# Optimization experiments

Measured on AMD Instinct MI355X. Metric: run time of the kernel, lower is better.

## Reference

```python
import jax, jax.numpy as jnp
import numpy as np

T = 2048      # num_tokens == max_seq_len
D = 4096      # d_in
H = 32        # num_heads
G = 8         # num_kv_groups
HD = 128      # head_dim
GS = H // G   # group_size = 4
EPS = 1e-6


def _make_rope(t, hd):
    inv_freq = 1.0 / (10000.0 ** (np.arange(0, hd, 2, dtype=np.float64) / hd))
    freqs = np.outer(np.arange(t, dtype=np.float64), inv_freq)      # [T, HD/2]
    emb = np.concatenate([freqs, freqs], axis=-1)                   # [T, HD]
    return (jnp.asarray(np.cos(emb), jnp.float32),
            jnp.asarray(np.sin(emb), jnp.float32))


def setup_inputs() -> dict:
    key = jax.random.key(0)
    ks = jax.random.split(key, 6)
    x = jax.random.normal(ks[0], (T, D), jnp.float32)
    # causal mask: True = masked (upper triangle above diagonal)
    mask = jnp.triu(jnp.ones((T, T), jnp.bool_), k=1)
    cos, sin = _make_rope(T, HD)
    s = 0.02
    Wq = jax.random.normal(ks[1], (D, H * HD), jnp.float32) * s
    Wk = jax.random.normal(ks[2], (D, G * HD), jnp.float32) * s
    Wv = jax.random.normal(ks[3], (D, G * HD), jnp.float32) * s
    Wo = jax.random.normal(ks[4], (H * HD, D), jnp.float32) * s
    qn_w = jnp.ones((HD,), jnp.float32)
    kn_w = jnp.ones((HD,), jnp.float32)
    return {"x": x, "mask": mask, "cos": cos, "sin": sin,
            "Wq": Wq, "Wk": Wk, "Wv": Wv, "Wo": Wo,
            "qn_w": qn_w, "kn_w": kn_w}


def _rmsnorm(u, w):
    # normalize over head_dim (last axis), eps inside sqrt
    var = jnp.mean(jnp.square(u), axis=-1, keepdims=True)
    return u * jax.lax.rsqrt(var + EPS) * w


def _rope(u, cos, sin):
    # rotate-half RoPE; u: [heads, T, HD], cos/sin: [T, HD]
    hd = u.shape[-1]
    u1, u2 = u[..., : hd // 2], u[..., hd // 2:]
    rot = jnp.concatenate([-u2, u1], axis=-1)
    return u * cos[None] + rot * sin[None]


def reference(x, mask, cos, sin, Wq, Wk, Wv, Wo, qn_w, kn_w):
    t = x.shape[0]
    q = (x @ Wq).reshape(t, H, HD).transpose(1, 0, 2)   # [H, T, HD]
    k = (x @ Wk).reshape(t, G, HD).transpose(1, 0, 2)   # [G, T, HD]
    v = (x @ Wv).reshape(t, G, HD).transpose(1, 0, 2)   # [G, T, HD]
    q = _rmsnorm(q, qn_w)
    k = _rmsnorm(k, kn_w)
    q = _rope(q, cos, sin)
    k = _rope(k, cos, sin)
    # GQA expansion: repeat_interleave along head axis
    k = jnp.repeat(k, GS, axis=0)                       # [H, T, HD]
    v = jnp.repeat(v, GS, axis=0)                       # [H, T, HD]
    scores = jnp.einsum('hqd,hkd->hqk', q, k) / (HD ** 0.5)
    scores = jnp.where(mask[None], -jnp.inf, scores)
    w = jax.nn.softmax(scores, axis=-1)
    attn = jnp.einsum('hqk,hkd->hqd', w, v)             # [H, T, HD]
    attn = attn.transpose(1, 0, 2).reshape(t, H * HD)
    return attn @ Wo
```

## Files before the change

### kernel.cpp

```cpp
#include <hip/hip_runtime.h>

#define T_ 2048
#define D_ 4096
#define H_ 32
#define G_ 8
#define HD_ 128

typedef float f32x4 __attribute__((ext_vector_type(4)));
typedef __bf16 bf16x8 __attribute__((ext_vector_type(8)));
typedef unsigned short u16x8 __attribute__((ext_vector_type(8)));
typedef unsigned short u16x4 __attribute__((ext_vector_type(4)));

__device__ __forceinline__ unsigned short f2bf(float f) {
  unsigned u = __builtin_bit_cast(unsigned, f);
  u += 0x7FFFu + ((u >> 16) & 1u);
  return (unsigned short)(u >> 16);
}
__device__ __forceinline__ float bf2f(unsigned short h) {
  return __builtin_bit_cast(float, (unsigned)h << 16);
}

__device__ __forceinline__ void gload_lds16(const unsigned short* g, unsigned short* l) {
  __builtin_amdgcn_global_load_lds((const __attribute__((address_space(1))) void*)g,
                                   (__attribute__((address_space(3))) void*)l, 16, 0, 0);
}

__global__ __launch_bounds__(256) void convert_bf16(const float* __restrict__ in,
                                                    unsigned short* __restrict__ out) {
  const size_t i = ((size_t)blockIdx.x * 256 + threadIdx.x) * 8;
  float4 a = *(const float4*)(in + i);
  float4 b = *(const float4*)(in + i + 4);
  u16x8 o;
  o[0] = f2bf(a.x); o[1] = f2bf(a.y); o[2] = f2bf(a.z); o[3] = f2bf(a.w);
  o[4] = f2bf(b.x); o[5] = f2bf(b.y); o[6] = f2bf(b.z); o[7] = f2bf(b.w);
  *(u16x8*)(out + i) = o;
}

__global__ __launch_bounds__(256) void transpose_convert(const float* __restrict__ Wm,
                                                         unsigned short* __restrict__ Wt,
                                                         int R, int C) {
  __shared__ float tile[64][65];
  const int r0 = blockIdx.x * 64, c0 = blockIdx.y * 64;
  const int lr4 = threadIdx.x >> 6, lc = threadIdx.x & 63;
#pragma unroll
  for (int i = 0; i < 16; ++i) {
    int r = i * 4 + lr4;
    tile[r][lc] = Wm[(size_t)(r0 + r) * C + c0 + lc];
  }
  __syncthreads();
#pragma unroll
  for (int i = 0; i < 16; ++i) {
    int r = i * 4 + lr4;
    Wt[(size_t)(c0 + r) * R + r0 + lc] = f2bf(tile[lc][r]);
  }
}

__global__ __launch_bounds__(256) void transpose_v(const unsigned short* __restrict__ v,
                                                   unsigned short* __restrict__ vt, int stride) {
  __shared__ unsigned short tile[64][65];
  const int t0 = blockIdx.x * 64, d0 = blockIdx.y * 64, g = blockIdx.z;
  const int lr4 = threadIdx.x >> 6, lc = threadIdx.x & 63;
#pragma unroll
  for (int i = 0; i < 16; ++i) {
    int r = i * 4 + lr4;
    tile[r][lc] = v[(size_t)(t0 + r) * stride + g * HD_ + d0 + lc];
  }
  __syncthreads();
#pragma unroll
  for (int i = 0; i < 16; ++i) {
    int r = i * 4 + lr4;
    vt[((size_t)g * HD_ + d0 + r) * T_ + t0 + lc] = tile[lc][r];
  }
}

__global__ __launch_bounds__(256) void norm_rope(const unsigned short* __restrict__ raw,
                                                 int stride,
                                                 unsigned short* __restrict__ outp,
                                                 const float* __restrict__ w,
                                                 const float* __restrict__ cs,
                                                 const float* __restrict__ sn, int NH) {
  const int row = blockIdx.x * 4 + (threadIdx.x >> 6);
  const int lane = threadIdx.x & 63;
  const int t = row / NH, h = row - t * NH;
  const unsigned short* src = raw + (size_t)t * stride + h * HD_;
  float u1 = bf2f(src[lane]);
  float u2 = bf2f(src[lane + 64]);
  float ss = u1 * u1 + u2 * u2;
#pragma unroll
  for (int m = 1; m < 64; m <<= 1) ss += __shfl_xor(ss, m);
  float rr = rsqrtf(ss * (1.f / 128.f) + 1e-6f);
  float c = cs[(size_t)t * HD_ + lane];
  float s = sn[(size_t)t * HD_ + lane];
  float a = u1 * rr * w[lane];
  float b = u2 * rr * w[lane + 64];
  unsigned short* dst = outp + ((size_t)h * T_ + t) * HD_;
  dst[lane]      = f2bf(a * c - b * s);
  dst[lane + 64] = f2bf(b * c + a * s);
}

template <int NF, int MQ, int F0, int F1>
__device__ __forceinline__ void mfma_g(f32x4 (&acc)[2][4][NF], bf16x8 (&af)[4][2],
                                       bf16x8 (&bf)[NF][2]) {
  __builtin_amdgcn_s_setprio(1);
#pragma unroll
  for (int fm = 0; fm < 4; ++fm)
#pragma unroll
    for (int fn = F0; fn < F1; ++fn) {
      f32x4 a = acc[MQ][fm][fn];
      a = __builtin_amdgcn_mfma_f32_16x16x32_bf16(af[fm][0], bf[fn][0], a, 0, 0, 0);
      a = __builtin_amdgcn_mfma_f32_16x16x32_bf16(af[fm][1], bf[fn][1], a, 0, 0, 0);
      acc[MQ][fm][fn] = a;
    }
  __builtin_amdgcn_s_setprio(0);
}

template <int NF, int OUTF32>
__global__ __launch_bounds__(512, 2) void gemm2(const unsigned short* __restrict__ A,
                                                const unsigned short* __restrict__ Bt,
                                                void* __restrict__ Cv, int M, int N,
                                                int K, int LDA) {
  constexpr int BN = NF * 64;
  constexpr int BBUF = NF * 4096;
  __shared__ __align__(16) unsigned short lds[32768 + 2 * BBUF];
  const int tid = threadIdx.x;
  const int wid = tid >> 6, lane = tid & 63;
  const int lr = lane & 15, lhi = lane >> 4;
  const int wr = wid >> 2, wcn = wid & 3;
  const int wr64 = wr * 64;

  int flat = blockIdx.y * gridDim.x + blockIdx.x;
  int nwg = gridDim.x * gridDim.y;
  int swz = (flat & 7) * (nwg >> 3) + (flat >> 3);
  const int brow = (swz & 7) * 256;
  const int bcol = (swz >> 3) * BN;

  const int nt = K >> 6;

  f32x4 acc[2][4][NF];
#pragma unroll
  for (int a = 0; a < 2; ++a)
#pragma unroll
    for (int b = 0; b < 4; ++b)
#pragma unroll
      for (int c = 0; c < NF; ++c) acc[a][b][c] = (f32x4){0.f, 0.f, 0.f, 0.f};

  const int t8 = tid >> 3;
  const int srcCol = ((tid & 7) ^ (t8 & 7)) * 8;
  auto stageA = [&](int d, int u, int ktp) {
    gload_lds16(A + (size_t)(brow + u * 64 + t8) * LDA + ktp * 64 + srcCol,
                &lds[d * 16384 + u * 4096 + tid * 8]);
  };
  auto stageB = [&](int d, int v, int ktp) {
    gload_lds16(Bt + (size_t)(bcol + v * 64 + t8) * LDA + ktp * 64 + srcCol,
                &lds[32768 + d * BBUF + v * 4096 + tid * 8]);
  };

  bf16x8 af[4][2], bf[NF][2];
  auto readA = [&](int d, int mq) {
#pragma unroll
    for (int fm = 0; fm < 4; ++fm) {
      int row = mq * 128 + wr64 + fm * 16 + lr;
      int base = d * 16384 + row * 64;
      int sw = (row & 7) << 3;
      af[fm][0] = *(const bf16x8*)&lds[base + ((lhi * 8) ^ sw)];
      af[fm][1] = *(const bf16x8*)&lds[base + ((32 + lhi * 8) ^ sw)];
    }
  };
  auto readBf = [&](int d, int fn, bf16x8 (&slot)[2]) {
    int row = wcn * (16 * NF) + fn * 16 + lr;
    int base = 32768 + d * BBUF + row * 64;
    int sw = (row & 7) << 3;
    slot[0] = *(const bf16x8*)&lds[base + ((lhi * 8) ^ sw)];
    slot[1] = *(const bf16x8*)&lds[base + ((32 + lhi * 8) ^ sw)];
  };

  stageA(0, 0, 0); stageA(0, 1, 0); stageA(0, 2, 0); stageA(0, 3, 0);
#pragma unroll
  for (int v = 0; v < NF; ++v) stageB(0, v, 0);
  stageA(1, 0, 1); stageA(1, 1, 1);
  asm volatile("s_waitcnt vmcnt(2)" ::: "memory");
  __builtin_amdgcn_s_barrier();

  for (int t = 0; t < nt; ++t) {
    const int d = t & 1, dn = d ^ 1;
    if constexpr (NF == 2) {
      readA(d, 0); readBf(d, 0, bf[0]); readBf(d, 1, bf[1]);
      if (t + 1 < nt) { stageA(dn, 2, t + 1); stageA(dn, 3, t + 1);
                        stageB(dn, 0, t + 1); stageB(dn, 1, t + 1); }
      __builtin_amdgcn_s_barrier();
      mfma_g<NF, 0, 0, 2>(acc, af, bf);
      __builtin_amdgcn_s_barrier();
      readA(d, 1);
      if (t + 2 < nt) { stageA(d, 0, t + 2); stageA(d, 1, t + 2); }
      __builtin_amdgcn_s_barrier();
      mfma_g<NF, 1, 0, 2>(acc, af, bf);
      if (t < nt - 2) asm volatile("s_waitcnt vmcnt(2)" ::: "memory");
      else if (t == nt - 2) asm volatile("s_waitcnt vmcnt(0)" ::: "memory");
      __builtin_amdgcn_s_barrier();
    } else {
      readA(d, 0); readBf(d, 0, bf[0]); readBf(d, 1, bf[1]);
      if (t + 1 < nt) { stageA(dn, 2, t + 1); stageA(dn, 3, t + 1); }
      __builtin_amdgcn_s_barrier();
      mfma_g<NF, 0, 0, 2>(acc, af, bf);
      __builtin_amdgcn_s_barrier();
      readBf(d, 2, bf[2]);
      if (t + 1 < nt) { stageB(dn, 0, t + 1); stageB(dn, 1, t + 1); stageB(dn, 2, t + 1); }
      __builtin_amdgcn_s_barrier();
      mfma_g<NF, 0, 2, 3>(acc, af, bf);
      __builtin_amdgcn_s_barrier();
      readA(d, 1);
      if (t + 2 < nt) { stageA(d, 0, t + 2); stageA(d, 1, t + 2); }
      __builtin_amdgcn_s_barrier();
      mfma_g<NF, 1, 0, 2>(acc, af, bf);
      __builtin_amdgcn_s_barrier();
      mfma_g<NF, 1, 2, 3>(acc, af, bf);
      if (t < nt - 2) asm volatile("s_waitcnt vmcnt(2)" ::: "memory");
      else if (t == nt - 2) asm volatile("s_waitcnt vmcnt(0)" ::: "memory");
      __builtin_amdgcn_s_barrier();
    }
  }

#pragma unroll
  for (int mq = 0; mq < 2; ++mq)
#pragma unroll
    for (int fm = 0; fm < 4; ++fm)
#pragma unroll
      for (int fn = 0; fn < NF; ++fn) {
        int col = bcol + wcn * (16 * NF) + fn * 16 + lr;
#pragma unroll
        for (int r = 0; r < 4; ++r) {
          int row = brow + mq * 128 + wr64 + fm * 16 + lhi * 4 + r;
          if (OUTF32)
            ((float*)Cv)[(size_t)row * N + col] = acc[mq][fm][fn][r];
          else
            ((unsigned short*)Cv)[(size_t)row * N + col] = f2bf(acc[mq][fm][fn][r]);
        }
      }
}

__global__ __launch_bounds__(512) void flash_attn(const unsigned short* __restrict__ q,
                                                  const unsigned short* __restrict__ k,
                                                  const unsigned short* __restrict__ vt,
                                                  unsigned short* __restrict__ attnb) {
  const int pairIdx = blockIdx.y;
  const int g = pairIdx >> 1;
  const int qc = gridDim.x - 1 - blockIdx.x;
  const int tid = threadIdx.x;
  const int wid = tid >> 6;
  const int lane = tid & 63;
  const int lr = lane & 15, lhi = lane >> 4;
  const int h = pairIdx * 2 + (wid >> 2);
  const int q0 = qc * 64 + (wid & 3) * 16;

  __shared__ __align__(16) unsigned short Ks[2][64 * HD_];
  __shared__ __align__(16) unsigned short Vs[2][HD_ * 64];
  __shared__ __align__(16) unsigned short p_lds_all[8][16 * 64];
  unsigned short* p_lds = p_lds_all[wid];

  const unsigned short* kg = k + (size_t)g * T_ * HD_;
  const unsigned short* vg = vt + (size_t)g * HD_ * T_;

  int ko[2], vo[2];
#pragma unroll
  for (int p = 0; p < 2; ++p) {
    int ob = (p * 512 + tid) * 16;
    int krow = ob >> 8, kb = ob & 255;
    ko[p] = krow * HD_ + ((kb ^ ((krow & 7) << 4)) >> 1);
    int vrow = ob >> 7, vb2 = ob & 127;
    vo[p] = vrow * T_ + ((vb2 ^ ((vrow & 7) << 4)) >> 1);
  }
  const int lbase = wid * 512;

  const int sx = (lr & 7) << 4;
  const float scale2 = 0.08838834764831845f * 1.4426950408889634f;

  bf16x8 qf[4];
  {
    const unsigned short* qrow = q + ((size_t)h * T_ + q0 + lr) * HD_ + lhi * 8;
#pragma unroll
    for (int c = 0; c < 4; ++c) qf[c] = *(const bf16x8*)(qrow + c * 32);
  }
  f32x4 accO[8];
#pragma unroll
  for (int i = 0; i < 8; ++i) accO[i] = (f32x4){0.f, 0.f, 0.f, 0.f};
  float mrow = -3e38f;
  float lrow = 0.f;

  const int ntile = qc + 1;

#pragma unroll
  for (int p = 0; p < 2; ++p) {
    gload_lds16(kg + ko[p], &Ks[0][p * 4096 + lbase]);
    gload_lds16(vg + vo[p], &Vs[0][p * 4096 + lbase]);
  }
  __syncthreads();

  for (int kt = 0; kt < ntile; ++kt) {
    const int b = kt & 1;
    const int kv0 = kt << 6;
    if (kt + 1 < ntile) {
      const size_t kofs = (size_t)(kv0 + 64) * HD_;
#pragma unroll
      for (int p = 0; p < 2; ++p) {
        gload_lds16(kg + kofs + ko[p], &Ks[b ^ 1][p * 4096 + lbase]);
        gload_lds16(vg + (kv0 + 64) + vo[p], &Vs[b ^ 1][p * 4096 + lbase]);
      }
    }
    f32x4 st[4];
    __builtin_amdgcn_s_setprio(1);
#pragma unroll
    for (int j = 0; j < 4; ++j) {
      st[j] = (f32x4){0.f, 0.f, 0.f, 0.f};
      const int krow = j * 16 + lr;
#pragma unroll
      for (int c = 0; c < 4; ++c) {
        bf16x8 kf = *(const bf16x8*)&Ks[b][krow * HD_ + (((c * 64 + lhi * 16) ^ sx) >> 1)];
        st[j] = __builtin_amdgcn_mfma_f32_16x16x32_bf16(kf, qf[c], st[j], 0, 0, 0);
      }
    }
    __builtin_amdgcn_s_setprio(0);
    if (kt == ntile - 1) {
#pragma unroll
      for (int j = 0; j < 4; ++j)
#pragma unroll
        for (int r = 0; r < 4; ++r)
          st[j][r] = (kv0 + j * 16 + lhi * 4 + r <= q0 + lr) ? st[j][r] * scale2 : -3e38f;
    } else {
#pragma unroll
      for (int j = 0; j < 4; ++j)
#pragma unroll
        for (int r = 0; r < 4; ++r) st[j][r] *= scale2;
    }
    float pm = st[0][0];
#pragma unroll
    for (int j = 0; j < 4; ++j)
#pragma unroll
      for (int r = 0; r < 4; ++r) pm = fmaxf(pm, st[j][r]);
    pm = fmaxf(pm, __shfl_xor(pm, 16));
    pm = fmaxf(pm, __shfl_xor(pm, 32));
    if (!__all(pm - mrow <= 8.f)) {
      float mnew = fmaxf(mrow, pm);
      float al = __builtin_amdgcn_exp2f(mrow - mnew);
      mrow = mnew;
      lrow *= al;
      float a0 = __shfl(al, lhi * 4 + 0);
      float a1 = __shfl(al, lhi * 4 + 1);
      float a2 = __shfl(al, lhi * 4 + 2);
      float a3 = __shfl(al, lhi * 4 + 3);
#pragma unroll
      for (int dt = 0; dt < 8; ++dt) {
        accO[dt][0] *= a0; accO[dt][1] *= a1; accO[dt][2] *= a2; accO[dt][3] *= a3;
      }
    }
    float ps = 0.f;
#pragma unroll
    for (int j = 0; j < 4; ++j)
#pragma unroll
      for (int r = 0; r < 4; ++r) {
        float e = __builtin_amdgcn_exp2f(st[j][r] - mrow);
        st[j][r] = e;
        ps += e;
      }
    ps += __shfl_xor(ps, 16);
    ps += __shfl_xor(ps, 32);
    lrow += ps;
#pragma unroll
    for (int j = 0; j < 4; ++j) {
      u16x4 pw;
      pw[0] = f2bf(st[j][0]); pw[1] = f2bf(st[j][1]);
      pw[2] = f2bf(st[j][2]); pw[3] = f2bf(st[j][3]);
      *(u16x4*)&p_lds[lr * 64 + (((j * 32 + lhi * 8) ^ sx) >> 1)] = pw;
    }
    bf16x8 pa0 = *(const bf16x8*)&p_lds[lr * 64 + (((lhi * 16) ^ sx) >> 1)];
    bf16x8 pa1 = *(const bf16x8*)&p_lds[lr * 64 + (((64 + lhi * 16) ^ sx) >> 1)];
    __builtin_amdgcn_s_setprio(1);
#pragma unroll
    for (int dt = 0; dt < 8; ++dt) {
      const int vrow = dt * 16 + lr;
      bf16x8 vf0 = *(const bf16x8*)&Vs[b][vrow * 64 + (((lhi * 16) ^ sx) >> 1)];
      bf16x8 vf1 = *(const bf16x8*)&Vs[b][vrow * 64 + (((64 + lhi * 16) ^ sx) >> 1)];
      accO[dt] = __builtin_amdgcn_mfma_f32_16x16x32_bf16(pa0, vf0, accO[dt], 0, 0, 0);
      accO[dt] = __builtin_amdgcn_mfma_f32_16x16x32_bf16(pa1, vf1, accO[dt], 0, 0, 0);
    }
    __builtin_amdgcn_s_setprio(0);
    __syncthreads();
  }
  float rinv = 1.f / lrow;
  float i0 = __shfl(rinv, lhi * 4 + 0);
  float i1 = __shfl(rinv, lhi * 4 + 1);
  float i2 = __shfl(rinv, lhi * 4 + 2);
  float i3 = __shfl(rinv, lhi * 4 + 3);
  float iv[4] = {i0, i1, i2, i3};
#pragma unroll
  for (int r = 0; r < 4; ++r) {
    size_t rowoff = (size_t)(q0 + lhi * 4 + r) * (H_ * HD_) + h * HD_;
#pragma unroll
    for (int dt = 0; dt < 8; ++dt) attnb[rowoff + dt * 16 + lr] = f2bf(accO[dt][r] * iv[r]);
  }
}

extern "C" void kernel_launch(void* const* d_in, const int* in_sizes, int n_in,
                              void* d_out, int out_size, void* d_ws, size_t ws_size,
                              hipStream_t stream) {
  const float* x = (const float*)d_in[0];
  const float* cosT = (const float*)d_in[2];
  const float* sinT = (const float*)d_in[3];
  const float* Wq = (const float*)d_in[4];
  const float* Wk = (const float*)d_in[5];
  const float* Wv = (const float*)d_in[6];
  const float* Wo = (const float*)d_in[7];
  const float* qn = (const float*)d_in[8];
  const float* kn = (const float*)d_in[9];

  unsigned char* w = (unsigned char*)d_ws;
  unsigned short* xb     = (unsigned short*)(w);
  unsigned short* WqkvT  = (unsigned short*)(w + 16777216);
  unsigned short* qkvraw = (unsigned short*)(w + 67108864);
  unsigned short* qbuf   = (unsigned short*)(w + 92274688);
  unsigned short* kbuf   = (unsigned short*)(w + 109051904);
  unsigned short* vtb    = (unsigned short*)(w + 113246208);
  unsigned short* WoT    = WqkvT;
  unsigned short* attnb  = xb;

  convert_bf16<<<dim3(4096), dim3(256), 0, stream>>>(x, xb);
  transpose_convert<<<dim3(64, 64), dim3(256), 0, stream>>>(Wq, WqkvT, 4096, 4096);
  transpose_convert<<<dim3(64, 16), dim3(256), 0, stream>>>(Wk, WqkvT + (size_t)4096 * 4096, 4096, 1024);
  transpose_convert<<<dim3(64, 16), dim3(256), 0, stream>>>(Wv, WqkvT + (size_t)5120 * 4096, 4096, 1024);

  gemm2<3, 0><<<dim3(8, 32), dim3(512), 0, stream>>>(xb, WqkvT, (void*)qkvraw, 2048, 6144, 4096, 4096);

  norm_rope<<<dim3(16384), dim3(256), 0, stream>>>(qkvraw, 6144, qbuf, qn, cosT, sinT, H_);
  norm_rope<<<dim3(4096), dim3(256), 0, stream>>>(qkvraw + 4096, 6144, kbuf, kn, cosT, sinT, G_);
  transpose_v<<<dim3(32, 2, 8), dim3(256), 0, stream>>>(qkvraw + 5120, vtb, 6144);
  transpose_convert<<<dim3(64, 64), dim3(256), 0, stream>>>(Wo, WoT, 4096, 4096);

  flash_attn<<<dim3(32, 16), dim3(512), 0, stream>>>(qbuf, kbuf, vtb, attnb);

  gemm2<2, 1><<<dim3(8, 32), dim3(512), 0, stream>>>(attnb, WoT, d_out, 2048, 4096, 4096, 4096);
}
```

Measured before the change: 350.2 us.

## Halve GEMM M-tile to 128 rows, doubling grid and occupancy

The GEMM kernel now computes 128-row output tiles instead of 256. That halves the accumulator registers and the A-tile LDS buffers, so the launch bound can rise to 4 blocks per CU and the grid doubles to 512 blocks. The aim is better latency hiding and fuller use of the CUs. In exchange, each B tile is reloaded twice as often and the arithmetic intensity per block drops. The pipeline schedule is rewritten to fit the single A sub-tile.

```diff
diff --git a/kernel.cpp b/kernel.cpp
--- a/kernel.cpp
+++ b/kernel.cpp
@@ -98,69 +98,66 @@
   dst[lane + 64] = f2bf(b * c + a * s);
 }
 
-template <int NF, int MQ, int F0, int F1>
-__device__ __forceinline__ void mfma_g(f32x4 (&acc)[2][4][NF], bf16x8 (&af)[4][2],
+template <int NF, int F0, int F1>
+__device__ __forceinline__ void mfma_g(f32x4 (&acc)[4][NF], bf16x8 (&af)[4][2],
                                        bf16x8 (&bf)[NF][2]) {
   __builtin_amdgcn_s_setprio(1);
 #pragma unroll
   for (int fm = 0; fm < 4; ++fm)
 #pragma unroll
     for (int fn = F0; fn < F1; ++fn) {
-      f32x4 a = acc[MQ][fm][fn];
+      f32x4 a = acc[fm][fn];
       a = __builtin_amdgcn_mfma_f32_16x16x32_bf16(af[fm][0], bf[fn][0], a, 0, 0, 0);
       a = __builtin_amdgcn_mfma_f32_16x16x32_bf16(af[fm][1], bf[fn][1], a, 0, 0, 0);
-      acc[MQ][fm][fn] = a;
+      acc[fm][fn] = a;
     }
   __builtin_amdgcn_s_setprio(0);
 }
 
 template <int NF, int OUTF32>
-__global__ __launch_bounds__(512, 2) void gemm2(const unsigned short* __restrict__ A,
+__global__ __launch_bounds__(512, 4) void gemm3(const unsigned short* __restrict__ A,
                                                 const unsigned short* __restrict__ Bt,
                                                 void* __restrict__ Cv, int M, int N,
                                                 int K, int LDA) {
   constexpr int BN = NF * 64;
   constexpr int BBUF = NF * 4096;
-  __shared__ __align__(16) unsigned short lds[32768 + 2 * BBUF];
+  __shared__ __align__(16) unsigned short lds[16384 + 2 * BBUF];
   const int tid = threadIdx.x;
   const int wid = tid >> 6, lane = tid & 63;
   const int lr = lane & 15, lhi = lane >> 4;
   const int wr = wid >> 2, wcn = wid & 3;
-  const int wr64 = wr * 64;
 
   int flat = blockIdx.y * gridDim.x + blockIdx.x;
   int nwg = gridDim.x * gridDim.y;
   int swz = (flat & 7) * (nwg >> 3) + (flat >> 3);
-  const int brow = (swz & 7) * 256;
-  const int bcol = (swz >> 3) * BN;
+  const int brow = (swz & 15) * 128;
+  const int bcol = (swz >> 4) * BN;
 
   const int nt = K >> 6;
 
-  f32x4 acc[2][4][NF];
-#pragma unroll
-  for (int a = 0; a < 2; ++a)
-#pragma unroll
-    for (int b = 0; b < 4; ++b)
-#pragma unroll
-      for (int c = 0; c < NF; ++c) acc[a][b][c] = (f32x4){0.f, 0.f, 0.f, 0.f};
+  f32x4 acc[4][NF];
+#pragma unroll
+  for (int b = 0; b < 4; ++b)
+#pragma unroll
+    for (int c = 0; c < NF; ++c) acc[b][c] = (f32x4){0.f, 0.f, 0.f, 0.f};
 
   const int t8 = tid >> 3;
   const int srcCol = ((tid & 7) ^ (t8 & 7)) * 8;
   auto stageA = [&](int d, int u, int ktp) {
     gload_lds16(A + (size_t)(brow + u * 64 + t8) * LDA + ktp * 64 + srcCol,
-                &lds[d * 16384 + u * 4096 + tid * 8]);
+                &lds[d * 8192 + u * 4096 + tid * 8]);
   };
   auto stageB = [&](int d, int v, int ktp) {
     gload_lds16(Bt + (size_t)(bcol + v * 64 + t8) * LDA + ktp * 64 + srcCol,
-                &lds[32768 + d * BBUF + v * 4096 + tid * 8]);
+                &lds[16384 + d * BBUF + v * 4096 + tid * 8]);
   };
 
   bf16x8 af[4][2], bf[NF][2];
-  auto readA = [&](int d, int mq) {
+  auto readA = [&](int d) {
 #pragma unroll
     for (int fm = 0; fm < 4; ++fm) {
-      int row = mq * 128 + wr64 + fm * 16 + lr;
-      int base = d * 16384 + row * 64;
+      int row = wr * 64 + fm * 16 + lr;
+      int base = d * 8192 + row * 64;
       int sw = (row & 7) << 3;
       af[fm][0] = *(const bf16x8*)&lds[base + ((lhi * 8) ^ sw)];
       af[fm][1] = *(const bf16x8*)&lds[base + ((32 + lhi * 8) ^ sw)];
@@ -168,13 +165,13 @@
   };
   auto readBf = [&](int d, int fn, bf16x8 (&slot)[2]) {
     int row = wcn * (16 * NF) + fn * 16 + lr;
-    int base = 32768 + d * BBUF + row * 64;
+    int base = 16384 + d * BBUF + row * 64;
     int sw = (row & 7) << 3;
     slot[0] = *(const bf16x8*)&lds[base + ((lhi * 8) ^ sw)];
     slot[1] = *(const bf16x8*)&lds[base + ((32 + lhi * 8) ^ sw)];
   };
 
-  stageA(0, 0, 0); stageA(0, 1, 0); stageA(0, 2, 0); stageA(0, 3, 0);
+  stageA(0, 0, 0); stageA(0, 1, 0);
 #pragma unroll
   for (int v = 0; v < NF; ++v) stageB(0, v, 0);
   stageA(1, 0, 1); stageA(1, 1, 1);
@@ -183,37 +180,29 @@
 
   for (int t = 0; t < nt; ++t) {
     const int d = t & 1, dn = d ^ 1;
-    if constexpr (NF == 2) {
-      readA(d, 0); readBf(d, 0, bf[0]); readBf(d, 1, bf[1]);
-      if (t + 1 < nt) { stageA(dn, 2, t + 1); stageA(dn, 3, t + 1);
-                        stageB(dn, 0, t + 1); stageB(dn, 1, t + 1); }
-      __builtin_amdgcn_s_barrier();
-      mfma_g<NF, 0, 0, 2>(acc, af, bf);
-      __builtin_amdgcn_s_barrier();
-      readA(d, 1);
+    if constexpr (NF == 3) {
+      readA(d); readBf(d, 0, bf[0]); readBf(d, 1, bf[1]);
+      if (t + 1 < nt) { stageB(dn, 0, t + 1); stageB(dn, 1, t + 1); stageB(dn, 2, t + 1); }
+      __builtin_amdgcn_s_barrier();
+      mfma_g<NF, 0, 2>(acc, af, bf);
+      __builtin_amdgcn_s_barrier();
+      readBf(d, 2, bf[2]);
       if (t + 2 < nt) { stageA(d, 0, t + 2); stageA(d, 1, t + 2); }
       __builtin_amdgcn_s_barrier();
-      mfma_g<NF, 1, 0, 2>(acc, af, bf);
+      mfma_g<NF, 2, 3>(acc, af, bf);
       if (t < nt - 2) asm volatile("s_waitcnt vmcnt(2)" ::: "memory");
       else if (t == nt - 2) asm volatile("s_waitcnt vmcnt(0)" ::: "memory");
       __builtin_amdgcn_s_barrier();
     } else {
-      readA(d, 0); readBf(d, 0, bf[0]); readBf(d, 1, bf[1]);
-      if (t + 1 < nt) { stageA(dn, 2, t + 1); stageA(dn, 3, t + 1); }
-      __builtin_amdgcn_s_barrier();
-      mfma_g<NF, 0, 0, 2>(acc, af, bf);
-      __builtin_amdgcn_s_barrier();
-      readBf(d, 2, bf[2]);
-      if (t + 1 < nt) { stageB(dn, 0, t + 1); stageB(dn, 1, t + 1); stageB(dn, 2, t + 1); }
-      __builtin_amdgcn_s_barrier();
-      mfma_g<NF, 0, 2, 3>(acc, af, bf);
-      __builtin_amdgcn_s_barrier();
-      readA(d, 1);
+      readA(d); readBf(d, 0, bf[0]);
+      if (t + 1 < nt) { stageB(dn, 0, t + 1); stageB(dn, 1, t + 1); }
+      __builtin_amdgcn_s_barrier();
+      mfma_g<NF, 0, 1>(acc, af, bf);
+      __builtin_amdgcn_s_barrier();
+      readBf(d, 1, bf[1]);
       if (t + 2 < nt) { stageA(d, 0, t + 2); stageA(d, 1, t + 2); }
       __builtin_amdgcn_s_barrier();
-      mfma_g<NF, 1, 0, 2>(acc, af, bf);
-      __builtin_amdgcn_s_barrier();
-      mfma_g<NF, 1, 2, 3>(acc, af, bf);
+      mfma_g<NF, 1, 2>(acc, af, bf);
       if (t < nt - 2) asm volatile("s_waitcnt vmcnt(2)" ::: "memory");
       else if (t == nt - 2) asm volatile("s_waitcnt vmcnt(0)" ::: "memory");
       __builtin_amdgcn_s_barrier();
@@ -221,21 +210,19 @@
   }
 
 #pragma unroll
-  for (int mq = 0; mq < 2; ++mq)
-#pragma unroll
-    for (int fm = 0; fm < 4; ++fm)
-#pragma unroll
-      for (int fn = 0; fn < NF; ++fn) {
-        int col = bcol + wcn * (16 * NF) + fn * 16 + lr;
-#pragma unroll
-        for (int r = 0; r < 4; ++r) {
-          int row = brow + mq * 128 + wr64 + fm * 16 + lhi * 4 + r;
-          if (OUTF32)
-            ((float*)Cv)[(size_t)row * N + col] = acc[mq][fm][fn][r];
-          else
-            ((unsigned short*)Cv)[(size_t)row * N + col] = f2bf(acc[mq][fm][fn][r]);
-        }
+  for (int fm = 0; fm < 4; ++fm)
+#pragma unroll
+    for (int fn = 0; fn < NF; ++fn) {
+      int col = bcol + wcn * (16 * NF) + fn * 16 + lr;
+#pragma unroll
+      for (int r = 0; r < 4; ++r) {
+        int row = brow + wr * 64 + fm * 16 + lhi * 4 + r;
+        if (OUTF32)
+          ((float*)Cv)[(size_t)row * N + col] = acc[fm][fn][r];
+        else
+          ((unsigned short*)Cv)[(size_t)row * N + col] = f2bf(acc[fm][fn][r]);
       }
+    }
 }
 
 __global__ __launch_bounds__(512) void flash_attn(const unsigned short* __restrict__ q,
@@ -427,7 +414,7 @@
   transpose_convert<<<dim3(64, 16), dim3(256), 0, stream>>>(Wk, WqkvT + (size_t)4096 * 4096, 4096, 1024);
   transpose_convert<<<dim3(64, 16), dim3(256), 0, stream>>>(Wv, WqkvT + (size_t)5120 * 4096, 4096, 1024);
 
-  gemm2<3, 0><<<dim3(8, 32), dim3(512), 0, stream>>>(xb, WqkvT, (void*)qkvraw, 2048, 6144, 4096, 4096);
+  gemm3<3, 0><<<dim3(16, 32), dim3(512), 0, stream>>>(xb, WqkvT, (void*)qkvraw, 2048, 6144, 4096, 4096);
 
   norm_rope<<<dim3(16384), dim3(256), 0, stream>>>(qkvraw, 6144, qbuf, qn, cosT, sinT, H_);
   norm_rope<<<dim3(4096), dim3(256), 0, stream>>>(qkvraw + 4096, 6144, kbuf, kn, cosT, sinT, G_);
@@ -436,5 +423,5 @@
 
   flash_attn<<<dim3(32, 16), dim3(512), 0, stream>>>(qbuf, kbuf, vtb, attnb);
 
-  gemm2<2, 1><<<dim3(8, 32), dim3(512), 0, stream>>>(attnb, WoT, d_out, 2048, 4096, 4096, 4096);
-}
+  gemm3<2, 1><<<dim3(16, 32), dim3(512), 0, stream>>>(attnb, WoT, d_out, 2048, 4096, 4096, 4096);
+}
```

Result: no change. 352.8 us (+0.8%).
